# Optimization experiments

Hardware: AMD Instinct MI355X
Metric: run time of the kernel (lower is better)

The kernel has to match this reference:

```python
import jax, jax.numpy as jnp
import numpy as np

N, D, K = 65536, 256, 4096  # tokens, code dim, codebook size


def setup_inputs() -> dict:
    key = jax.random.key(0)
    kx, kc = jax.random.split(key)
    x = jax.random.normal(kx, (N, D), dtype=jnp.float32)
    # variance_scaling(1.0, fan_in, uniform): limit = sqrt(3/fan_in), fan_in = D
    limit = float(np.sqrt(3.0 / D))
    codebook = jax.random.uniform(kc, (K, D), dtype=jnp.float32, minval=-limit, maxval=limit)
    return {"x": x, "codebook": codebook}


def reference(x, codebook):
    orig_shape = x.shape
    flat = jnp.reshape(x, (-1, codebook.shape[-1]))                 # [N, D]
    a2 = jnp.sum(flat * flat, axis=-1, keepdims=True)               # [N, 1]
    b2 = jnp.sum(codebook * codebook, axis=-1)[None, :]             # [1, K]
    # squared L2 distance via ||a||^2 + ||b||^2 - 2 a.b
    dist = a2 + b2 - 2.0 * jnp.matmul(flat, codebook.T)             # [N, K]
    idx = jnp.argmin(dist, axis=-1)                                 # [N]
    z_q = codebook[idx]                                             # [N, D] gather
    # straight-through estimator
    z_q = flat + jax.lax.stop_gradient(z_q - flat)
    return jnp.reshape(z_q, orig_shape)
```

## Files before the change

kernel.cpp:

```cpp
#include <hip/hip_runtime.h>
#include <cstdint>

typedef _Float16 f16;
typedef __attribute__((ext_vector_type(8)))  f16   v8h;
typedef __attribute__((ext_vector_type(16))) float v16f;
typedef __attribute__((ext_vector_type(4)))  float v4f;
typedef unsigned short ushort_t;

#define N_TOK  65536
#define DIM    256
#define K_CB   4096
#define BN     128
#define NCHUNK 128
#define MARGIN_S  3.0e-3f
#define MARGIN_S2 2.0e-4f

#define MFMA(a,b,c) __builtin_amdgcn_mfma_f32_32x32x16_f16(a,b,c,0,0,0)
#define MED3(a,b,c) __builtin_amdgcn_fmed3f(a,b,c)

static __device__ __forceinline__ v4f ntload4(const void* p) {
    return __builtin_nontemporal_load((const v4f*)p);
}
static __device__ __forceinline__ void ntstore4(void* p, v4f v) {
    __builtin_nontemporal_store(v, (v4f*)p);
}

static __device__ __forceinline__ int decode_k(float p, int wid, int lhalf) {
    unsigned tag = __float_as_uint(p) & 255u;
    int kci = tag >> 5, m = (tag >> 4) & 1, r = tag & 15;
    return (kci << 9) + wid * 64 + 4 * lhalf + (m << 5) + (r & 3) + 8 * (r >> 2);
}

static __device__ __forceinline__ void merge5(float& s1, int& i1, float& s2, int& i2, float& s3,
                                              float o1, int oi1, float o2, int oi2, float o3) {
    bool aw = s1 >= o1;
    float w1 = aw ? s1 : o1;  int wi1 = aw ? i1 : oi1;
    float w2 = aw ? s2 : o2;  int wi2 = aw ? i2 : oi2;
    float w3 = aw ? s3 : o3;
    float l1 = aw ? o1 : s1;  int li1 = aw ? oi1 : i1;
    float l2 = aw ? o2 : s2;
    bool c = l1 > w2;
    s1 = w1; i1 = wi1;
    s2 = c ? l1 : w2; i2 = c ? li1 : wi2;
    s3 = c ? fmaxf(w2, l2) : fmaxf(w3, l1);
}

__global__ void pack_cb(const float* __restrict__ cb, ushort_t* __restrict__ cbh,
                        ushort_t* __restrict__ cbl, float* __restrict__ b2,
                        int* __restrict__ cnts) {
    __shared__ float red[256];
    int tid = threadIdx.x;
    if (blockIdx.x == 0 && tid < 4) cnts[tid] = 0;
    int gid = blockIdx.x * 256 + tid;
    int k = gid >> 5, grp = gid & 31;
    int ci = grp >> 1, khalf = grp & 1;
    int kci = k >> 9, c = k & 511;
    int wav = c >> 6, cloc = c & 63;
    const float* src = cb + (size_t)k * DIM + grp * 8;
    float4 v0 = *(const float4*)(src);
    float4 v1 = *(const float4*)(src + 4);
    float f[8] = {v0.x, v0.y, v0.z, v0.w, v1.x, v1.y, v1.z, v1.w};
    v8h hv, lv;
    float ss = 0.f;
#pragma unroll
    for (int e = 0; e < 8; ++e) {
        f16 h = (f16)f[e];
        hv[e] = h;
        lv[e] = (f16)(f[e] - (float)h);
        ss = fmaf(f[e], f[e], ss);
    }
    size_t base = ((size_t)(kci * 16 + ci)) * 8192 + wav * 1024 + khalf * 512 + cloc * 8;
    *(v8h*)(cbh + base) = hv;
    *(v8h*)(cbl + base) = lv;
    red[tid] = ss;
    __syncthreads();
#pragma unroll
    for (int s = 16; s > 0; s >>= 1) {
        if ((tid & 31) < s) red[tid] += red[tid + s];
        __syncthreads();
    }
    if ((tid & 31) == 0) b2[gid >> 5] = red[tid];
}

__global__ __launch_bounds__(512, 2) void argmin_kernel(
    const float* __restrict__ x, const ushort_t* __restrict__ cbh,
    const float* __restrict__ b2, int* __restrict__ bestIdx,
    int* __restrict__ cnts, int* __restrict__ flagList, int* __restrict__ liteList)
{
    __shared__ __align__(16) f16   Xh[32 * 128 * 8];
    __shared__ __align__(16) float B2s[K_CB];

    const int tid   = threadIdx.x;
    const int wid   = tid >> 6;
    const int lane  = tid & 63;
    const int l31   = lane & 31;
    const int lhalf = lane >> 5;
    const int n0    = blockIdx.x * BN;

    {
        const int token = tid >> 2, dseg = tid & 3;
        const float* xr = x + (size_t)(n0 + token) * DIM + dseg * 64;
#pragma unroll
        for (int sgrp = 0; sgrp < 8; ++sgrp) {
            v4f a = ntload4(xr + 8 * sgrp);
            v4f b = ntload4(xr + 8 * sgrp + 4);
            float f[8] = {a.x, a.y, a.z, a.w, b.x, b.y, b.z, b.w};
            v8h hv;
#pragma unroll
            for (int e = 0; e < 8; ++e) hv[e] = (f16)f[e];
            *(v8h*)(Xh + ((dseg * 8 + sgrp) * 128 + token) * 8) = hv;
        }
        const int o = tid * 8;
        *(float4*)(B2s + o)     = *(const float4*)(b2 + o);
        *(float4*)(B2s + o + 4) = *(const float4*)(b2 + o + 4);
    }
    __syncthreads();

    const ushort_t* ap = cbh + (size_t)wid * 1024 + (size_t)lhalf * 512 + (size_t)l31 * 8;

#define LOAD_A(A, g_) do { \
        const ushort_t* p_ = ap + (size_t)(g_) * 8192; \
        A##0 = *(const v8h*)(p_); A##1 = *(const v8h*)(p_ + 256); } while (0)
#define READ_B(B, g_) do { \
        int boff_ = ((((g_) & 15) * 2 + lhalf) * 128 + l31) * 8; \
        B##0 = *(const v8h*)(Xh + boff_);       B##1 = *(const v8h*)(Xh + boff_ + 256); \
        B##2 = *(const v8h*)(Xh + boff_ + 512); B##3 = *(const v8h*)(Xh + boff_ + 768); } while (0)
#define MFMA8(A, B) do { \
        acc[0][0] = MFMA(A##0, B##0, acc[0][0]); \
        acc[0][1] = MFMA(A##0, B##1, acc[0][1]); \
        acc[0][2] = MFMA(A##0, B##2, acc[0][2]); \
        acc[0][3] = MFMA(A##0, B##3, acc[0][3]); \
        acc[1][0] = MFMA(A##1, B##0, acc[1][0]); \
        acc[1][1] = MFMA(A##1, B##1, acc[1][1]); \
        acc[1][2] = MFMA(A##1, B##2, acc[1][2]); \
        acc[1][3] = MFMA(A##1, B##3, acc[1][3]); } while (0)

    v16f vzero;
#pragma unroll
    for (int r = 0; r < 16; ++r) vzero[r] = 0.0f;
    v16f acc[2][4];
#pragma unroll
    for (int a = 0; a < 2; ++a)
#pragma unroll
        for (int b = 0; b < 4; ++b) acc[a][b] = vzero;

    float b1d[4], b2d[4], b3d[4];
#pragma unroll
    for (int j = 0; j < 4; ++j) {
        b1d[j] = -3.0e38f; b2d[j] = -3.0e38f; b3d[j] = -3.0e38f;
    }

    v8h Aa0, Aa1, Ab0, Ab1;
    v8h Ba0, Ba1, Ba2, Ba3, Bb0, Bb1, Bb2, Bb3;

    LOAD_A(Aa, 0); READ_B(Ba, 0);
    LOAD_A(Ab, 1); READ_B(Bb, 1);

#pragma unroll 1
    for (int g = 0; g < NCHUNK; g += 2) {
        MFMA8(Aa, Ba);
        { int gp = (g + 2 < NCHUNK) ? g + 2 : 0; LOAD_A(Aa, gp); READ_B(Ba, gp); }
        MFMA8(Ab, Bb);
        { int gp = (g + 3 < NCHUNK) ? g + 3 : 0; LOAD_A(Ab, gp); READ_B(Bb, gp); }

        if ((g & 15) == 14) {
            const int kci = g >> 4;
            const int bbase = (kci << 9) + wid * 64 + 4 * lhalf;
            const unsigned tagk = (unsigned)(kci << 5);
#pragma unroll
            for (int m = 0; m < 2; ++m) {
                const float* bp = B2s + bbase + m * 32;
                float4 q0 = *(const float4*)(bp);
                float4 q1 = *(const float4*)(bp + 8);
                float4 q2 = *(const float4*)(bp + 16);
                float4 q3 = *(const float4*)(bp + 24);
                float bw[16] = {q0.x, q0.y, q0.z, q0.w, q1.x, q1.y, q1.z, q1.w,
                                q2.x, q2.y, q2.z, q2.w, q3.x, q3.y, q3.z, q3.w};
#pragma unroll
                for (int j = 0; j < 4; ++j) {
#pragma unroll
                    for (int r = 0; r < 16; ++r) {
                        float sv = fmaf(-0.5f, bw[r], acc[m][j][r]);
                        unsigned tag = tagk | (unsigned)((m << 4) | r);
                        float pk = __uint_as_float((__float_as_uint(sv) & 0xFFFFFF00u) | tag);
                        b3d[j] = MED3(pk, b2d[j], b3d[j]);
                        b2d[j] = MED3(pk, b1d[j], b2d[j]);
                        b1d[j] = fmaxf(b1d[j], pk);
                    }
                    acc[m][j] = vzero;
                }
            }
        }
    }

    int b1i[4], b2i[4];
#pragma unroll
    for (int j = 0; j < 4; ++j) {
        b1i[j] = decode_k(b1d[j], wid, lhalf);
        b2i[j] = decode_k(b2d[j], wid, lhalf);
    }
#pragma unroll
    for (int j = 0; j < 4; ++j) {
        float o1 = __shfl_xor(b1d[j], 32);
        float o2 = __shfl_xor(b2d[j], 32);
        float o3 = __shfl_xor(b3d[j], 32);
        int  oi1 = __shfl_xor(b1i[j], 32);
        int  oi2 = __shfl_xor(b2i[j], 32);
        merge5(b1d[j], b1i[j], b2d[j], b2i[j], b3d[j], o1, oi1, o2, oi2, o3);
    }

    __syncthreads();
    float* f1  = (float*)Xh;
    float* f2  = f1 + 1024;
    float* f3  = f2 + 1024;
    int*   fi1 = (int*)(f3 + 1024);
    int*   fi2 = fi1 + 1024;
    if (lane < 32) {
#pragma unroll
        for (int j = 0; j < 4; ++j) {
            int idx = wid * 128 + j * 32 + l31;
            f1[idx] = b1d[j]; f2[idx] = b2d[j]; f3[idx] = b3d[j];
            fi1[idx] = b1i[j]; fi2[idx] = b2i[j];
        }
    }
    __syncthreads();
    if (tid < BN) {
        float s1 = -3.0e38f, s2 = -3.0e38f, s3 = -3.0e38f;
        int i1 = 0x7fffffff, i2 = 0x7fffffff;
#pragma unroll
        for (int w = 0; w < 8; ++w) {
            int idx = w * 128 + tid;
            merge5(s1, i1, s2, i2, s3, f1[idx], fi1[idx], f2[idx], fi2[idx], f3[idx]);
        }
        int n = n0 + tid;
        bestIdx[n] = i1;
        if (s1 - s2 < MARGIN_S) {
            if (s1 - s3 < MARGIN_S) {
                int pos = atomicAdd(&cnts[0], 1);
                flagList[pos] = n;
            } else {
                int pos = atomicAdd(&cnts[2], 1);
                liteList[pos] = (n << 12) | i2;
            }
        }
    }
}

__global__ __launch_bounds__(256) void refine_lite(
    const float* __restrict__ x, const float* __restrict__ cb,
    const int* __restrict__ cnts, const int* __restrict__ liteList,
    int* __restrict__ bestIdx)
{
    const int tid = threadIdx.x;
    const int w = tid >> 6, lane = tid & 63, l31 = lane & 31;
    const int cnt3 = cnts[2];
    for (int t = blockIdx.x * 4 + w; t < cnt3; t += gridDim.x * 4) {
        const int ent = liteList[t];
        const int n = ent >> 12, i2 = ent & 4095;
        const int i1 = bestIdx[n];
        const int code = (lane < 32) ? i1 : i2;
        const float* cr = cb + (size_t)code * DIM + l31 * 8;
        const float* xr = x + (size_t)n * DIM + l31 * 8;
        double s = 0.0;
#pragma unroll
        for (int d = 0; d < 8; ++d) {
            double c = cr[d];
            s += c * (c - 2.0 * (double)xr[d]);
        }
#pragma unroll
        for (int off = 1; off < 32; off <<= 1) s += __shfl_xor(s, off, 64);
        double so = __shfl_xor(s, 32, 64);
        if (lane == 0) {
            bestIdx[n] = (so < s || (so == s && i2 < i1)) ? i2 : i1;
        }
    }
}

__global__ __launch_bounds__(512) void refine1_kernel(
    const float* __restrict__ x, const ushort_t* __restrict__ cbh,
    const ushort_t* __restrict__ cbl, const float* __restrict__ b2,
    const int* __restrict__ cnts, const int* __restrict__ flagList,
    float* __restrict__ ps1, float* __restrict__ ps2, int* __restrict__ pidx)
{
    __shared__ __align__(16) f16   Xh[32 * 32 * 8];
    __shared__ __align__(16) f16   Xl[32 * 32 * 8];
    __shared__ __align__(16) float B2q[1024];

    const int tid   = threadIdx.x;
    const int wid   = tid >> 6;
    const int lane  = tid & 63;
    const int l31   = lane & 31;
    const int lhalf = lane >> 5;
    const int grpI  = blockIdx.x >> 2;
    const int qid   = blockIdx.x & 3;
    const int cnt   = cnts[0];
    const int f0    = grpI * 32;
    if (f0 >= cnt) return;

    {
        const int token = tid >> 4, dseg = tid & 15;
        const int f = f0 + token;
        const int n = (f < cnt) ? flagList[f] : 0;
        const float* xr = x + (size_t)n * DIM + dseg * 16;
#pragma unroll
        for (int s = 0; s < 2; ++s) {
            v4f a = ntload4(xr + 8 * s);
            v4f b = ntload4(xr + 8 * s + 4);
            float f8[8] = {a.x, a.y, a.z, a.w, b.x, b.y, b.z, b.w};
            v8h hv, lv;
#pragma unroll
            for (int e = 0; e < 8; ++e) {
                f16 h = (f16)f8[e];
                hv[e] = h; lv[e] = (f16)(f8[e] - (float)h);
            }
            int grp = dseg * 2 + s;
            *(v8h*)(Xh + (grp * 32 + token) * 8) = hv;
            *(v8h*)(Xl + (grp * 32 + token) * 8) = lv;
        }
        if (tid < 256) *(float4*)(B2q + tid * 4) = *(const float4*)(b2 + qid * 1024 + tid * 4);
    }
    __syncthreads();

    const size_t qoff = (size_t)qid * 32 * 8192;
    const size_t loff = (size_t)wid * 1024 + (size_t)lhalf * 512 + (size_t)l31 * 8;
    const ushort_t* aph = cbh + qoff + loff;
    const ushort_t* apl = cbl + qoff + loff;

#define LOAD_A6(H0_, H1_, L0_, L1_, g_) do { \
        const ushort_t* ph_ = aph + (size_t)(g_) * 8192; \
        const ushort_t* pl_ = apl + (size_t)(g_) * 8192; \
        H0_ = *(const v8h*)(ph_); H1_ = *(const v8h*)(ph_ + 256); \
        L0_ = *(const v8h*)(pl_); L1_ = *(const v8h*)(pl_ + 256); } while (0)
#define READ_B6(BH_, BL_, g_) do { \
        int boff_ = ((((g_) & 15) * 2 + lhalf) * 32 + l31) * 8; \
        BH_ = *(const v8h*)(Xh + boff_); BL_ = *(const v8h*)(Xl + boff_); } while (0)
#define MFMA6(H0_, H1_, L0_, L1_, BH_, BL_) do { \
        acc0 = MFMA(H0_, BH_, acc0); acc1 = MFMA(H1_, BH_, acc1); \
        acc0 = MFMA(H0_, BL_, acc0); acc1 = MFMA(H1_, BL_, acc1); \
        acc0 = MFMA(L0_, BH_, acc0); acc1 = MFMA(L1_, BH_, acc1); } while (0)

    v16f vzero;
#pragma unroll
    for (int r = 0; r < 16; ++r) vzero[r] = 0.0f;
    v16f acc0 = vzero, acc1 = vzero;
    float b1d = -3.0e38f, b2d = -3.0e38f; int b1i = 0x7fffffff;

    v8h Ha0, Ha1, La0, La1, Hb0, Hb1, Lb0, Lb1;
    v8h BHa, BLa, BHb, BLb;

    LOAD_A6(Ha0, Ha1, La0, La1, 0); READ_B6(BHa, BLa, 0);
    LOAD_A6(Hb0, Hb1, Lb0, Lb1, 1); READ_B6(BHb, BLb, 1);

#pragma unroll 1
    for (int gl = 0; gl < 32; gl += 2) {
        MFMA6(Ha0, Ha1, La0, La1, BHa, BLa);
        { int gp = (gl + 2 < 32) ? gl + 2 : 0; LOAD_A6(Ha0, Ha1, La0, La1, gp); READ_B6(BHa, BLa, gp); }
        MFMA6(Hb0, Hb1, Lb0, Lb1, BHb, BLb);
        { int gp = (gl + 3 < 32) ? gl + 3 : 0; LOAD_A6(Hb0, Hb1, Lb0, Lb1, gp); READ_B6(BHb, BLb, gp); }

        if ((gl & 15) == 14) {
            const int kci_l = gl >> 4;
            const int bb_l  = (kci_l << 9) + wid * 64 + 4 * lhalf;
#pragma unroll
            for (int m = 0; m < 2; ++m) {
                const float* bp = B2q + bb_l + m * 32;
                float4 q0 = *(const float4*)(bp);
                float4 q1 = *(const float4*)(bp + 8);
                float4 q2 = *(const float4*)(bp + 16);
                float4 q3 = *(const float4*)(bp + 24);
                float bw[16] = {q0.x, q0.y, q0.z, q0.w, q1.x, q1.y, q1.z, q1.w,
                                q2.x, q2.y, q2.z, q2.w, q3.x, q3.y, q3.z, q3.w};
                const int kbase = qid * 1024 + bb_l + m * 32;
                v16f a = (m == 0) ? acc0 : acc1;
#pragma unroll
                for (int r = 0; r < 16; ++r) {
                    float sv = fmaf(-0.5f, bw[r], a[r]);
                    int k = kbase + (r & 3) + 8 * (r >> 2);
                    bool better = sv > b1d;
                    b2d = MED3(sv, b1d, b2d);
                    b1d = fmaxf(b1d, sv);
                    b1i = better ? k : b1i;
                }
            }
            acc0 = vzero; acc1 = vzero;
        }
    }

    {
        float o1 = __shfl_xor(b1d, 32);
        float o2 = __shfl_xor(b2d, 32);
        int   oi = __shfl_xor(b1i, 32);
        bool ow = o1 > b1d;
        float nb2 = fmaxf(fminf(b1d, o1), fmaxf(b2d, o2));
        b1i = ow ? oi : b1i;
        b1d = fmaxf(b1d, o1);
        b2d = nb2;
    }
    __syncthreads();
    float* f1 = (float*)Xh;
    float* f2 = f1 + 256;
    int*   fi = (int*)(f2 + 256);
    if (lane < 32) {
        int idx = wid * 32 + l31;
        f1[idx] = b1d; f2[idx] = b2d; fi[idx] = b1i;
    }
    __syncthreads();
    if (tid < 32 && f0 + tid < cnt) {
        float s1 = -3.0e38f, s2 = -3.0e38f; int si = 0x7fffffff;
#pragma unroll
        for (int w = 0; w < 8; ++w) {
            float c1 = f1[w * 32 + tid], c2 = f2[w * 32 + tid];
            int  ci1 = fi[w * 32 + tid];
            bool ow = c1 > s1;
            float nb2 = fmaxf(fminf(s1, c1), fmaxf(s2, c2));
            si = ow ? ci1 : si; s1 = fmaxf(s1, c1); s2 = nb2;
        }
        const int f = f0 + tid;
        ps1 [qid * 65536 + f] = s1;
        ps2 [qid * 65536 + f] = s2;
        pidx[qid * 65536 + f] = si;
    }
}

__global__ void merge_kernel(int* __restrict__ cnts, const int* __restrict__ flagList,
                             const float* __restrict__ ps1, const float* __restrict__ ps2,
                             const int* __restrict__ pidx, int* __restrict__ bestIdx,
                             int* __restrict__ flagList2)
{
    const int cnt = cnts[0];
    for (int f = blockIdx.x * 256 + threadIdx.x; f < cnt; f += gridDim.x * 256) {
        float s1 = -3.0e38f, s2 = -3.0e38f; int si = 0x7fffffff;
#pragma unroll
        for (int q = 0; q < 4; ++q) {
            float c1 = ps1[q * 65536 + f], c2 = ps2[q * 65536 + f];
            int  ci1 = pidx[q * 65536 + f];
            bool ow = c1 > s1;
            float nb2 = fmaxf(fminf(s1, c1), fmaxf(s2, c2));
            si = ow ? ci1 : si; s1 = fmaxf(s1, c1); s2 = nb2;
        }
        const int n = flagList[f];
        bestIdx[n] = si;
        if (s1 - s2 < MARGIN_S2) {
            int pos = atomicAdd(&cnts[1], 1);
            flagList2[pos] = n;
        }
    }
}

__global__ __launch_bounds__(512) void refine2_kernel(
    const float* __restrict__ x, const float* __restrict__ cb,
    const int* __restrict__ cnts, const int* __restrict__ flagList2,
    int* __restrict__ bestIdx)
{
    __shared__ float  xr[DIM];
    __shared__ double rd[512];
    __shared__ int    ri[512];
    const int tid = threadIdx.x;
    const int cnt2 = cnts[1];
    for (int f = blockIdx.x; f < cnt2; f += gridDim.x) {
        const int n = flagList2[f];
        __syncthreads();
        if (tid < 64) {
            v4f v = ntload4(x + (size_t)n * DIM + tid * 4);
            xr[tid * 4 + 0] = v.x; xr[tid * 4 + 1] = v.y;
            xr[tid * 4 + 2] = v.z; xr[tid * 4 + 3] = v.w;
        }
        __syncthreads();
        double best = 1e300; int bi = 0x7fffffff;
#pragma unroll
        for (int grp = 0; grp < 2; ++grp) {
            const int k0 = grp * 2048 + tid;
            const float4* cr0 = reinterpret_cast<const float4*>(cb + (size_t)k0 * DIM);
            const float4* cr1 = reinterpret_cast<const float4*>(cb + (size_t)(k0 + 512) * DIM);
            const float4* cr2 = reinterpret_cast<const float4*>(cb + (size_t)(k0 + 1024) * DIM);
            const float4* cr3 = reinterpret_cast<const float4*>(cb + (size_t)(k0 + 1536) * DIM);
            double s0a = 0, s0b = 0, s1a = 0, s1b = 0;
            double s2a = 0, s2b = 0, s3a = 0, s3b = 0;
#pragma unroll 4
            for (int q = 0; q < 64; ++q) {
                float4 c0 = cr0[q], c1 = cr1[q], c2 = cr2[q], c3 = cr3[q];
                double x0 = xr[4 * q + 0], x1 = xr[4 * q + 1];
                double x2 = xr[4 * q + 2], x3 = xr[4 * q + 3];
                s0a += (double)c0.x * ((double)c0.x - 2.0 * x0) + (double)c0.y * ((double)c0.y - 2.0 * x1);
                s0b += (double)c0.z * ((double)c0.z - 2.0 * x2) + (double)c0.w * ((double)c0.w - 2.0 * x3);
                s1a += (double)c1.x * ((double)c1.x - 2.0 * x0) + (double)c1.y * ((double)c1.y - 2.0 * x1);
                s1b += (double)c1.z * ((double)c1.z - 2.0 * x2) + (double)c1.w * ((double)c1.w - 2.0 * x3);
                s2a += (double)c2.x * ((double)c2.x - 2.0 * x0) + (double)c2.y * ((double)c2.y - 2.0 * x1);
                s2b += (double)c2.z * ((double)c2.z - 2.0 * x2) + (double)c2.w * ((double)c2.w - 2.0 * x3);
                s3a += (double)c3.x * ((double)c3.x - 2.0 * x0) + (double)c3.y * ((double)c3.y - 2.0 * x1);
                s3b += (double)c3.z * ((double)c3.z - 2.0 * x2) + (double)c3.w * ((double)c3.w - 2.0 * x3);
            }
            double d0 = s0a + s0b, d1 = s1a + s1b, d2 = s2a + s2b, d3 = s3a + s3b;
            if (d0 < best || (d0 == best && k0        < bi)) { best = d0; bi = k0; }
            if (d1 < best || (d1 == best && k0 + 512  < bi)) { best = d1; bi = k0 + 512; }
            if (d2 < best || (d2 == best && k0 + 1024 < bi)) { best = d2; bi = k0 + 1024; }
            if (d3 < best || (d3 == best && k0 + 1536 < bi)) { best = d3; bi = k0 + 1536; }
        }
        rd[tid] = best; ri[tid] = bi;
        __syncthreads();
        for (int s = 256; s > 0; s >>= 1) {
            if (tid < s) {
                double od = rd[tid + s]; int oi = ri[tid + s];
                if (od < rd[tid] || (od == rd[tid] && oi < ri[tid])) { rd[tid] = od; ri[tid] = oi; }
            }
            __syncthreads();
        }
        if (tid == 0) bestIdx[n] = ri[0];
        __syncthreads();
    }
}

__global__ void gather_kernel(const float* __restrict__ cb, const int* __restrict__ bestIdx,
                              float* __restrict__ out)
{
    int t = blockIdx.x * 256 + threadIdx.x;
    int n = t >> 6, f4 = t & 63;
    int k = bestIdx[n];
    v4f v = *reinterpret_cast<const v4f*>(cb + (size_t)k * DIM + f4 * 4);
    ntstore4(out + (size_t)t * 4, v);
}

extern "C" void kernel_launch(void* const* d_in, const int* in_sizes, int n_in,
                              void* d_out, int out_size, void* d_ws, size_t ws_size,
                              hipStream_t stream)
{
    const float* x  = (const float*)d_in[0];
    const float* cb = (const float*)d_in[1];
    float* out = (float*)d_out;

    char* ws = (char*)d_ws;
    ushort_t* cbh      = (ushort_t*)ws;
    ushort_t* cbl      = (ushort_t*)(ws + 2097152);
    float*    b2       = (float*)(ws + 4194304);
    int*      bestIdx  = (int*)(ws + 4210688);
    int*      cnts     = (int*)(ws + 4472832);
    int*      flagList = (int*)(ws + 4472848);
    int*      flagList2= (int*)(ws + 4734992);
    float*    ps1      = (float*)(ws + 4997136);
    float*    ps2      = (float*)(ws + 6045712);
    int*      pidx     = (int*)(ws + 7094288);
    int*      liteList = (int*)ps1;

    pack_cb       <<<dim3(512),  dim3(256), 0, stream>>>(cb, cbh, cbl, b2, cnts);
    argmin_kernel <<<dim3(N_TOK / BN), dim3(512), 0, stream>>>(x, cbh, b2, bestIdx, cnts, flagList, liteList);
    refine_lite   <<<dim3(512),  dim3(256), 0, stream>>>(x, cb, cnts, liteList, bestIdx);
    refine1_kernel<<<dim3(8192), dim3(512), 0, stream>>>(x, cbh, cbl, b2, cnts, flagList, ps1, ps2, pidx);
    merge_kernel  <<<dim3(64),   dim3(256), 0, stream>>>(cnts, flagList, ps1, ps2, pidx, bestIdx, flagList2);
    refine2_kernel<<<dim3(1024), dim3(512), 0, stream>>>(x, cb, cnts, flagList2, bestIdx);
    gather_kernel <<<dim3(N_TOK * 64 / 256), dim3(256), 0, stream>>>(cb, bestIdx, out);
}
```

Measured before the change: 216.8 us.

## Fold codebook norm bias into MFMA via augmented K-chunk with ones vector

Result: slower. 224.1 us (+3.3%).

```diff
diff --git a/kernel.cpp b/kernel.cpp
--- a/kernel.cpp
+++ b/kernel.cpp
@@ -12,6 +12,7 @@
 #define K_CB   4096
 #define BN     128
 #define NCHUNK 128
+#define GMAP(g_) ((((g_) >> 4) * 17) + ((g_) & 15))
 #define MARGIN_S  3.0e-3f
 #define MARGIN_S2 2.0e-4f
 
@@ -69,9 +70,9 @@
         lv[e] = (f16)(f[e] - (float)h);
         ss = fmaf(f[e], f[e], ss);
     }
-    size_t base = ((size_t)(kci * 16 + ci)) * 8192 + wav * 1024 + khalf * 512 + cloc * 8;
-    *(v8h*)(cbh + base) = hv;
-    *(v8h*)(cbl + base) = lv;
+    size_t sub = (size_t)wav * 1024 + khalf * 512 + cloc * 8;
+    *(v8h*)(cbh + ((size_t)(kci * 17 + ci)) * 8192 + sub) = hv;
+    *(v8h*)(cbl + ((size_t)(kci * 16 + ci)) * 8192 + sub) = lv;
     red[tid] = ss;
     __syncthreads();
 #pragma unroll
@@ -82,13 +83,26 @@
     if ((tid & 31) == 0) b2[gid >> 5] = red[tid];
 }
 
+__global__ void pack_b2(const float* __restrict__ b2, ushort_t* __restrict__ cbh) {
+    int k = blockIdx.x * 256 + threadIdx.x;
+    if (k >= K_CB) return;
+    int kci = k >> 9, c = k & 511;
+    int wav = c >> 6, cloc = c & 63;
+    v8h hv, zv;
+#pragma unroll
+    for (int e = 0; e < 8; ++e) { hv[e] = (f16)0.0f; zv[e] = (f16)0.0f; }
+    hv[0] = (f16)(-0.5f * b2[k]);
+    size_t base = ((size_t)(kci * 17 + 16)) * 8192 + (size_t)wav * 1024 + (size_t)cloc * 8;
+    *(v8h*)(cbh + base)       = hv;
+    *(v8h*)(cbh + base + 512) = zv;
+}
+
 __global__ __launch_bounds__(512, 2) void argmin_kernel(
     const float* __restrict__ x, const ushort_t* __restrict__ cbh,
-    const float* __restrict__ b2, int* __restrict__ bestIdx,
-    int* __restrict__ cnts, int* __restrict__ flagList, int* __restrict__ liteList)
-{
-    __shared__ __align__(16) f16   Xh[32 * 128 * 8];
-    __shared__ __align__(16) float B2s[K_CB];
+    int* __restrict__ bestIdx, int* __restrict__ cnts,
+    int* __restrict__ flagList, int* __restrict__ liteList)
+{
+    __shared__ __align__(16) f16 Xh[32 * 128 * 8];
 
     const int tid   = threadIdx.x;
     const int wid   = tid >> 6;
@@ -110,16 +124,18 @@
             for (int e = 0; e < 8; ++e) hv[e] = (f16)f[e];
             *(v8h*)(Xh + ((dseg * 8 + sgrp) * 128 + token) * 8) = hv;
         }
-        const int o = tid * 8;
-        *(float4*)(B2s + o)     = *(const float4*)(b2 + o);
-        *(float4*)(B2s + o + 4) = *(const float4*)(b2 + o + 4);
-    }
-    __syncthreads();
+    }
+    __syncthreads();
+
+    v8h bones;
+#pragma unroll
+    for (int e = 0; e < 8; ++e) bones[e] = (f16)0.0f;
+    if (lhalf == 0) bones[0] = (f16)1.0f;
 
     const ushort_t* ap = cbh + (size_t)wid * 1024 + (size_t)lhalf * 512 + (size_t)l31 * 8;
 
-#define LOAD_A(A, g_) do { \
-        const ushort_t* p_ = ap + (size_t)(g_) * 8192; \
+#define LOAD_A(A, raw_) do { \
+        const ushort_t* p_ = ap + (size_t)(raw_) * 8192; \
         A##0 = *(const v8h*)(p_); A##1 = *(const v8h*)(p_ + 256); } while (0)
 #define READ_B(B, g_) do { \
         int boff_ = ((((g_) & 15) * 2 + lhalf) * 128 + l31) * 8; \
@@ -150,37 +166,40 @@
         b1d[j] = -3.0e38f; b2d[j] = -3.0e38f; b3d[j] = -3.0e38f;
     }
 
-    v8h Aa0, Aa1, Ab0, Ab1;
+    v8h Aa0, Aa1, Ab0, Ab1, Ac0, Ac1;
     v8h Ba0, Ba1, Ba2, Ba3, Bb0, Bb1, Bb2, Bb3;
 
-    LOAD_A(Aa, 0); READ_B(Ba, 0);
-    LOAD_A(Ab, 1); READ_B(Bb, 1);
+    LOAD_A(Aa, GMAP(0)); READ_B(Ba, 0);
+    LOAD_A(Ab, GMAP(1)); READ_B(Bb, 1);
 
 #pragma unroll 1
     for (int g = 0; g < NCHUNK; g += 2) {
         MFMA8(Aa, Ba);
-        { int gp = (g + 2 < NCHUNK) ? g + 2 : 0; LOAD_A(Aa, gp); READ_B(Ba, gp); }
+        { int gp = (g + 2 < NCHUNK) ? g + 2 : 0; LOAD_A(Aa, GMAP(gp)); READ_B(Ba, gp); }
         MFMA8(Ab, Bb);
-        { int gp = (g + 3 < NCHUNK) ? g + 3 : 0; LOAD_A(Ab, gp); READ_B(Bb, gp); }
-
+        { int gp = (g + 3 < NCHUNK) ? g + 3 : 0; LOAD_A(Ab, GMAP(gp)); READ_B(Bb, gp); }
+
+        if ((g & 15) == 12) {
+            LOAD_A(Ac, (g >> 4) * 17 + 16);
+        }
         if ((g & 15) == 14) {
             const int kci = g >> 4;
-            const int bbase = (kci << 9) + wid * 64 + 4 * lhalf;
+            acc[0][0] = MFMA(Ac0, bones, acc[0][0]);
+            acc[0][1] = MFMA(Ac0, bones, acc[0][1]);
+            acc[0][2] = MFMA(Ac0, bones, acc[0][2]);
+            acc[0][3] = MFMA(Ac0, bones, acc[0][3]);
+            acc[1][0] = MFMA(Ac1, bones, acc[1][0]);
+            acc[1][1] = MFMA(Ac1, bones, acc[1][1]);
+            acc[1][2] = MFMA(Ac1, bones, acc[1][2]);
+            acc[1][3] = MFMA(Ac1, bones, acc[1][3]);
             const unsigned tagk = (unsigned)(kci << 5);
 #pragma unroll
             for (int m = 0; m < 2; ++m) {
-                const float* bp = B2s + bbase + m * 32;
-                float4 q0 = *(const float4*)(bp);
-                float4 q1 = *(const float4*)(bp + 8);
-                float4 q2 = *(const float4*)(bp + 16);
-                float4 q3 = *(const float4*)(bp + 24);
-                float bw[16] = {q0.x, q0.y, q0.z, q0.w, q1.x, q1.y, q1.z, q1.w,
-                                q2.x, q2.y, q2.z, q2.w, q3.x, q3.y, q3.z, q3.w};
 #pragma unroll
                 for (int j = 0; j < 4; ++j) {
 #pragma unroll
                     for (int r = 0; r < 16; ++r) {
-                        float sv = fmaf(-0.5f, bw[r], acc[m][j][r]);
+                        float sv = acc[m][j][r];
                         unsigned tag = tagk | (unsigned)((m << 4) | r);
                         float pk = __uint_as_float((__float_as_uint(sv) & 0xFFFFFF00u) | tag);
                         b3d[j] = MED3(pk, b2d[j], b3d[j]);
@@ -321,14 +340,13 @@
     }
     __syncthreads();
 
-    const size_t qoff = (size_t)qid * 32 * 8192;
     const size_t loff = (size_t)wid * 1024 + (size_t)lhalf * 512 + (size_t)l31 * 8;
-    const ushort_t* aph = cbh + qoff + loff;
-    const ushort_t* apl = cbl + qoff + loff;
-
-#define LOAD_A6(H0_, H1_, L0_, L1_, g_) do { \
-        const ushort_t* ph_ = aph + (size_t)(g_) * 8192; \
-        const ushort_t* pl_ = apl + (size_t)(g_) * 8192; \
+    const ushort_t* aph = cbh + loff;
+    const ushort_t* apl = cbl + loff;
+
+#define LOAD_A6(H0_, H1_, L0_, L1_, d_) do { \
+        const ushort_t* ph_ = aph + (size_t)GMAP(d_) * 8192; \
+        const ushort_t* pl_ = apl + (size_t)(d_) * 8192; \
         H0_ = *(const v8h*)(ph_); H1_ = *(const v8h*)(ph_ + 256); \
         L0_ = *(const v8h*)(pl_); L1_ = *(const v8h*)(pl_ + 256); } while (0)
 #define READ_B6(BH_, BL_, g_) do { \
@@ -348,15 +366,15 @@
     v8h Ha0, Ha1, La0, La1, Hb0, Hb1, Lb0, Lb1;
     v8h BHa, BLa, BHb, BLb;
 
-    LOAD_A6(Ha0, Ha1, La0, La1, 0); READ_B6(BHa, BLa, 0);
-    LOAD_A6(Hb0, Hb1, Lb0, Lb1, 1); READ_B6(BHb, BLb, 1);
+    LOAD_A6(Ha0, Ha1, La0, La1, qid * 32 + 0); READ_B6(BHa, BLa, 0);
+    LOAD_A6(Hb0, Hb1, Lb0, Lb1, qid * 32 + 1); READ_B6(BHb, BLb, 1);
 
 #pragma unroll 1
     for (int gl = 0; gl < 32; gl += 2) {
         MFMA6(Ha0, Ha1, La0, La1, BHa, BLa);
-        { int gp = (gl + 2 < 32) ? gl + 2 : 0; LOAD_A6(Ha0, Ha1, La0, La1, gp); READ_B6(BHa, BLa, gp); }
+        { int gp = (gl + 2 < 32) ? gl + 2 : 0; LOAD_A6(Ha0, Ha1, La0, La1, qid * 32 + gp); READ_B6(BHa, BLa, gp); }
         MFMA6(Hb0, Hb1, Lb0, Lb1, BHb, BLb);
-        { int gp = (gl + 3 < 32) ? gl + 3 : 0; LOAD_A6(Hb0, Hb1, Lb0, Lb1, gp); READ_B6(BHb, BLb, gp); }
+        { int gp = (gl + 3 < 32) ? gl + 3 : 0; LOAD_A6(Hb0, Hb1, Lb0, Lb1, qid * 32 + gp); READ_B6(BHb, BLb, gp); }
 
         if ((gl & 15) == 14) {
             const int kci_l = gl >> 4;
@@ -530,19 +548,20 @@
 
     char* ws = (char*)d_ws;
     ushort_t* cbh      = (ushort_t*)ws;
-    ushort_t* cbl      = (ushort_t*)(ws + 2097152);
-    float*    b2       = (float*)(ws + 4194304);
-    int*      bestIdx  = (int*)(ws + 4210688);
-    int*      cnts     = (int*)(ws + 4472832);
-    int*      flagList = (int*)(ws + 4472848);
-    int*      flagList2= (int*)(ws + 4734992);
-    float*    ps1      = (float*)(ws + 4997136);
-    float*    ps2      = (float*)(ws + 6045712);
-    int*      pidx     = (int*)(ws + 7094288);
+    ushort_t* cbl      = (ushort_t*)(ws + 2228224);
+    float*    b2       = (float*)(ws + 4325376);
+    int*      bestIdx  = (int*)(ws + 4341760);
+    int*      cnts     = (int*)(ws + 4603904);
+    int*      flagList = (int*)(ws + 4603920);
+    int*      flagList2= (int*)(ws + 4866064);
+    float*    ps1      = (float*)(ws + 5128208);
+    float*    ps2      = (float*)(ws + 6176784);
+    int*      pidx     = (int*)(ws + 7225360);
     int*      liteList = (int*)ps1;
 
     pack_cb       <<<dim3(512),  dim3(256), 0, stream>>>(cb, cbh, cbl, b2, cnts);
-    argmin_kernel <<<dim3(N_TOK / BN), dim3(512), 0, stream>>>(x, cbh, b2, bestIdx, cnts, flagList, liteList);
+    pack_b2       <<<dim3(16),   dim3(256), 0, stream>>>(b2, cbh);
+    argmin_kernel <<<dim3(N_TOK / BN), dim3(512), 0, stream>>>(x, cbh, bestIdx, cnts, flagList, liteList);
     refine_lite   <<<dim3(512),  dim3(256), 0, stream>>>(x, cb, cnts, liteList, bestIdx);
     refine1_kernel<<<dim3(8192), dim3(512), 0, stream>>>(x, cbh, cbl, b2, cnts, flagList, ps1, ps2, pidx);
     merge_kernel  <<<dim3(64),   dim3(256), 0, stream>>>(cnts, flagList, ps1, ps2, pidx, bestIdx, flagList2);
```
